# Performance work log

Measured on AMD Instinct MI355X. Metric: run time of the kernel, lower is better.

## Reference

```python
import jax, jax.numpy as jnp
import numpy as np

B, S, E = 4, 2048, 1024

def setup_inputs() -> dict:
    key = jax.random.key(0)
    ks = jax.random.split(key, 7)
    sc = 1.0 / np.sqrt(E)
    return {
        "x": jax.random.normal(ks[0], (B, S, E), dtype=jnp.float32),
        "wq_w": jax.random.normal(ks[1], (E, E), dtype=jnp.float32) * sc,
        "wq_b": jax.random.normal(ks[2], (E,), dtype=jnp.float32) * 0.01,
        "wk_w": jax.random.normal(ks[3], (E, E), dtype=jnp.float32) * sc,
        "wk_b": jax.random.normal(ks[4], (E,), dtype=jnp.float32) * 0.01,
        "wv_w": jax.random.normal(ks[5], (E, E), dtype=jnp.float32) * sc,
        "wv_b": jax.random.normal(ks[6], (E,), dtype=jnp.float32) * 0.01,
    }

def reference(x, wq_w, wq_b, wk_w, wk_b, wv_w, wv_b):
    # Linear projections (torch nn.Linear: y = x @ W^T + b)
    Q = jnp.einsum('bse,fe->bsf', x, wq_w) + wq_b
    K = jnp.einsum('bse,fe->bsf', x, wk_w) + wk_b
    V = jnp.einsum('bse,fe->bsf', x, wv_w) + wv_b
    # scaled dot-product attention, full [B, S, S] scores (single head)
    scores = jnp.einsum('bqe,bke->bqk', Q, K) / jnp.sqrt(jnp.asarray(Q.shape[-1], Q.dtype))
    attn = jax.nn.softmax(scores, axis=-1)
    return jnp.einsum('bqk,bke->bqe', attn, V)
```

## Files before the change

### kernel.cpp

```cpp
#include <hip/hip_runtime.h>
#include <hip/hip_bf16.h>
#include <stdint.h>

#define B_ 4
#define S_ 2048
#define E_ 1024

typedef __bf16 bf16;
typedef __attribute__((ext_vector_type(8))) __bf16 bf16x8;
typedef __attribute__((ext_vector_type(4))) float f32x4;
typedef __attribute__((ext_vector_type(4))) float float4v;
typedef __attribute__((ext_vector_type(4))) unsigned int uint4v;
typedef __attribute__((ext_vector_type(4))) unsigned short ushort4v;

__device__ inline unsigned short f2bf(float f) {
  union { float f; unsigned int u; } c; c.f = f;
  unsigned int u = c.u;
  unsigned int r = (u + 0x7FFFu + ((u >> 16) & 1u)) >> 16;
  return (unsigned short)r;
}

__device__ inline void load16_to_lds(const void* g, void* l) {
  __builtin_amdgcn_global_load_lds(
      (const __attribute__((address_space(1))) void*)g,
      (__attribute__((address_space(3))) void*)l,
      16, 0, 0);
}

__global__ __launch_bounds__(256) void cvt_all(
    const float* __restrict__ x, const float* __restrict__ w0,
    const float* __restrict__ w1, const float* __restrict__ w2,
    unsigned short* __restrict__ out) {
  const long off = (long)blockIdx.x * 256 + threadIdx.x;
  const float* in;
  long ibase;
  if (blockIdx.x < 8192)       { in = x;  ibase = 0; }
  else if (blockIdx.x < 9216)  { in = w0; ibase = 8192L * 256; }
  else if (blockIdx.x < 10240) { in = w1; ibase = 9216L * 256; }
  else                         { in = w2; ibase = 10240L * 256; }
  float4v f = ((const float4v*)in)[off - ibase];
  ushort4v o;
  o.x = f2bf(f.x); o.y = f2bf(f.y); o.z = f2bf(f.z); o.w = f2bf(f.w);
  ((ushort4v*)out)[off] = o;
}

template <int MODE, int SWZ, int NXT>
__global__ __launch_bounds__(256, 4) void gemm_bt(
    const bf16* __restrict__ A, const bf16* __restrict__ B, void* __restrict__ Cv,
    const float* __restrict__ bias, const float* __restrict__ bias_b,
    const float* __restrict__ bias_v, unsigned short* __restrict__ VtOut,
    float* __restrict__ rowsum,
    int M, int N, int K, int lda, int ldb, int ldc,
    long sA, long sB, long sC, float scale, int nyt) {
  __shared__ bf16 As[128 * 64];
  __shared__ bf16 Bs[128 * 64];

  int xt, yt, zb;
  if (SWZ == 0) {
    xt = blockIdx.x; yt = blockIdx.y; zb = blockIdx.z;
  } else {
    const int flat = blockIdx.x;
    const int xcd = flat & 7;
    const int local = flat >> 3;
    zb = xcd >> 1;
    const int w = (xcd & 1) * (NXT * nyt / 2) + local;
    xt = w % NXT; yt = w / NXT;
  }

  A += (long)zb * sA;
  B += (long)zb * sB;
  const int tid = threadIdx.x;
  const int wave = tid >> 6;
  const int lane = tid & 63;
  const int lrow = lane & 15;
  const int quad = lane >> 4;
  const int row0 = yt * 128;
  const int col0 = xt * 128;
  const int wm = (wave >> 1) * 64;
  const int wn = (wave & 1) * 64;

  f32x4 acc[4][4] = {};

  const int r0 = wave * 8 + (lane >> 3);
  const int c0 = (lane & 7) * 8;

  const bf16* pA0 = A + (long)(row0 + r0) * lda + c0;
  const bf16* pA1 = pA0 + 32L * lda;
  const bf16* pA2 = pA0 + 64L * lda;
  const bf16* pA3 = pA0 + 96L * lda;
  const bf16* pB0 = B + (long)(col0 + r0) * ldb + c0;
  const bf16* pB1 = pB0 + 32L * ldb;
  const bf16* pB2 = pB0 + 64L * ldb;
  const bf16* pB3 = pB0 + 96L * ldb;
  bf16* ldsA = As + wave * 512;
  bf16* ldsB = Bs + wave * 512;

  for (int ks = 0; ks < K; ks += 64) {
    load16_to_lds(pA0, ldsA);
    load16_to_lds(pA1, ldsA + 2048);
    load16_to_lds(pA2, ldsA + 4096);
    load16_to_lds(pA3, ldsA + 6144);
    load16_to_lds(pB0, ldsB);
    load16_to_lds(pB1, ldsB + 2048);
    load16_to_lds(pB2, ldsB + 4096);
    load16_to_lds(pB3, ldsB + 6144);
    __syncthreads();
#pragma unroll
    for (int kk = 0; kk < 64; kk += 32) {
      bf16x8 af[4], bfr[4];
#pragma unroll
      for (int i = 0; i < 4; ++i)
        af[i] = *(const bf16x8*)(As + (wm + i * 16 + lrow) * 64 + kk + quad * 8);
#pragma unroll
      for (int j = 0; j < 4; ++j)
        bfr[j] = *(const bf16x8*)(Bs + (wn + j * 16 + lrow) * 64 + kk + quad * 8);
#pragma unroll
      for (int i = 0; i < 4; ++i)
#pragma unroll
        for (int j = 0; j < 4; ++j)
          acc[i][j] = __builtin_amdgcn_mfma_f32_16x16x32_bf16(af[i], bfr[j], acc[i][j], 0, 0, 0);
    }
    __syncthreads();
    pA0 += 64; pA1 += 64; pA2 += 64; pA3 += 64;
    pB0 += 64; pB1 += 64; pB2 += 64; pB3 += 64;
  }

  if (MODE == 8) {
    float* C = (float*)Cv + (long)zb * sC;
    const float* rs = rowsum + (long)zb * S_;
#pragma unroll
    for (int i = 0; i < 4; ++i) {
#pragma unroll
      for (int r = 0; r < 4; ++r) {
        const int row = row0 + wm + i * 16 + quad * 4 + r;
        const float inv = 1.0f / rs[row];
#pragma unroll
        for (int j = 0; j < 4; ++j) {
          const int col = col0 + wn + j * 16 + lrow;
          C[(long)row * ldc + col] = acc[i][j][r] * inv;
        }
      }
    }
  } else if (MODE == 7) {
    unsigned short* C = (unsigned short*)Cv + (long)zb * sC;
    float* rs = rowsum + (long)zb * S_;
    float rsump[4][4];
#pragma unroll
    for (int i = 0; i < 4; ++i)
#pragma unroll
      for (int r = 0; r < 4; ++r) rsump[i][r] = 0.f;
#pragma unroll
    for (int j = 0; j < 4; ++j) {
      const int col = col0 + wn + j * 16 + lrow;
#pragma unroll
      for (int i = 0; i < 4; ++i) {
#pragma unroll
        for (int r = 0; r < 4; ++r) {
          const int row = row0 + wm + i * 16 + quad * 4 + r;
          const float e = __expf(acc[i][j][r] * scale);
          rsump[i][r] += e;
          C[(long)row * ldc + col] = f2bf(e);
        }
      }
    }
#pragma unroll
    for (int i = 0; i < 4; ++i) {
#pragma unroll
      for (int r = 0; r < 4; ++r) {
        float v = rsump[i][r];
        v += __shfl_xor(v, 1);
        v += __shfl_xor(v, 2);
        v += __shfl_xor(v, 4);
        v += __shfl_xor(v, 8);
        if (lrow == 0)
          atomicAdd(&rs[row0 + wm + i * 16 + quad * 4 + r], v);
      }
    }
  } else {
    if (col0 < 2048) {
      unsigned short* C = (unsigned short*)Cv;
#pragma unroll
      for (int j = 0; j < 4; ++j) {
        const int col = col0 + wn + j * 16 + lrow;
        const float bcol = (col < E_) ? bias[col] : bias_b[col - E_];
#pragma unroll
        for (int i = 0; i < 4; ++i) {
#pragma unroll
          for (int r = 0; r < 4; ++r) {
            const int row = row0 + wm + i * 16 + quad * 4 + r;
            C[(long)row * ldc + col] = f2bf(acc[i][j][r] + bcol);
          }
        }
      }
    } else {
#pragma unroll
      for (int j = 0; j < 4; ++j) {
        const int e = col0 + wn + j * 16 + lrow - 2048;
        const float bv_ = bias_v[e];
#pragma unroll
        for (int i = 0; i < 4; ++i) {
          const int row = row0 + wm + i * 16 + quad * 4;
          ushort4v o;
          o.x = f2bf(acc[i][j][0] + bv_);
          o.y = f2bf(acc[i][j][1] + bv_);
          o.z = f2bf(acc[i][j][2] + bv_);
          o.w = f2bf(acc[i][j][3] + bv_);
          *(ushort4v*)(VtOut + (long)e * (B_ * S_) + row) = o;
        }
      }
    }
  }
}

extern "C" void kernel_launch(void* const* d_in, const int* in_sizes, int n_in,
                              void* d_out, int out_size, void* d_ws, size_t ws_size,
                              hipStream_t stream) {
  const float* x    = (const float*)d_in[0];
  const float* wq_w = (const float*)d_in[1];
  const float* wq_b = (const float*)d_in[2];
  const float* wk_w = (const float*)d_in[3];
  const float* wk_b = (const float*)d_in[4];
  const float* wv_w = (const float*)d_in[5];
  const float* wv_b = (const float*)d_in[6];
  float* out = (float*)d_out;

  const long NX = (long)B_ * S_ * E_;
  const long NW = (long)E_ * E_;
  char* ws = (char*)d_ws;
  bf16* xb  = (bf16*)ws; ws += NX * 2;
  bf16* wqb = (bf16*)ws; ws += NW * 2;
  bf16* wkb = (bf16*)ws; ws += NW * 2;
  bf16* wvb = (bf16*)ws; ws += NW * 2;
  bf16* QK  = (bf16*)ws; ws += 2 * NX * 2;
  bf16* Vt  = (bf16*)ws; ws += NX * 2;
  bf16* Sc  = (bf16*)ws; ws += (long)B_ * S_ * S_ * 2;
  float* rowsum = (float*)ws; ws += (long)B_ * S_ * 4;

  cvt_all<<<dim3(11264), 256, 0, stream>>>(
      x, wq_w, wk_w, wv_w, (unsigned short*)xb);
  hipMemsetAsync(rowsum, 0, (size_t)B_ * S_ * 4, stream);

  dim3 blk(256);
  gemm_bt<6, 0, 24><<<dim3((3 * E_) / 128, (B_ * S_) / 128, 1), blk, 0, stream>>>(
      xb, wqb, QK, wq_b, wk_b, wv_b, (unsigned short*)Vt, nullptr,
      B_ * S_, 3 * E_, E_, E_, E_, 2 * E_, 0, 0, 0, 1.f, 64);
  gemm_bt<7, 1, 16><<<dim3(1024, 1, 1), blk, 0, stream>>>(
      QK, QK + E_, Sc, nullptr, nullptr, nullptr, nullptr, rowsum,
      S_, S_, E_, 2 * E_, 2 * E_, S_,
      (long)S_ * 2 * E_, (long)S_ * 2 * E_, (long)S_ * S_, 0.03125f, 16);
  gemm_bt<8, 1, 8><<<dim3(512, 1, 1), blk, 0, stream>>>(
      Sc, Vt, out, nullptr, nullptr, nullptr, nullptr, rowsum,
      S_, E_, S_, S_, B_ * S_, E_,
      (long)S_ * S_, (long)S_, (long)S_ * E_, 1.f, 16);
}
```

Baseline: 256.6 us.

## Add 256x256 double-buffered swizzled-LDS GEMM kernel for projection and score stages

Introduces a new 512-thread GEMM kernel with 256x256 output tiles, a 128KB double-buffered LDS with XOR swizzle, and a four-phase pipelined k-loop. Each phase issues the next global-to-LDS loads while running MFMAs, using explicit vmcnt waits, barriers and setprio. The QKV projection and QK^T score GEMMs now use it, while the PV GEMM stays on the old kernel. Larger tiles cut global traffic and the pipelining hides load latency, but the grids shrink to 384 and 256 blocks, which risks leaving CUs idle and lowers occupancy.

```diff
diff --git a/kernel.cpp b/kernel.cpp
--- a/kernel.cpp
+++ b/kernel.cpp
@@ -44,6 +44,237 @@
   ((ushort4v*)out)[off] = o;
 }
 
+
+#define MFMA_(a, b, c) __builtin_amdgcn_mfma_f32_16x16x32_bf16(a, b, c, 0, 0, 0)
+
+#define STAGE_A8(kh, buf, kofs)                                         \
+  { char* d_ = smem + (buf) * 65536 + (kh) * 16384 + wj;                \
+    load16_to_lds(pA0 + (kofs) + (kh) * 32, d_);                        \
+    load16_to_lds(pA1 + (kofs) + (kh) * 32, d_ + 1024); }
+
+#define STAGE_B8(kh, buf, kofs)                                         \
+  { char* d_ = smem + (buf) * 65536 + 32768 + (kh) * 16384 + wj;        \
+    load16_to_lds(pB0 + (kofs) + (kh) * 32, d_);                        \
+    load16_to_lds(pB1 + (kofs) + (kh) * 32, d_ + 1024); }
+
+#define PH_READS(mh, kh)                                                \
+    const char* rb_ = smem + cur * 65536 + (kh) * 16384;                \
+    bf16x8 a0_ = *(const bf16x8*)(rb_ + offA[(mh) * 4 + 0]);            \
+    bf16x8 a1_ = *(const bf16x8*)(rb_ + offA[(mh) * 4 + 1]);            \
+    bf16x8 a2_ = *(const bf16x8*)(rb_ + offA[(mh) * 4 + 2]);            \
+    bf16x8 a3_ = *(const bf16x8*)(rb_ + offA[(mh) * 4 + 3]);            \
+    bf16x8 b0_ = *(const bf16x8*)(rb_ + offB[0]);                       \
+    bf16x8 b1_ = *(const bf16x8*)(rb_ + offB[1]);                       \
+    bf16x8 b2_ = *(const bf16x8*)(rb_ + offB[2]);                       \
+    bf16x8 b3_ = *(const bf16x8*)(rb_ + offB[3])
+
+#define PH_TAIL(mh)                                                     \
+    __builtin_amdgcn_s_barrier();                                       \
+    asm volatile("s_waitcnt lgkmcnt(0)" ::: "memory");                  \
+    __builtin_amdgcn_s_setprio(1);                                      \
+    acc[(mh)*4+0][0] = MFMA_(a0_, b0_, acc[(mh)*4+0][0]);               \
+    acc[(mh)*4+0][1] = MFMA_(a0_, b1_, acc[(mh)*4+0][1]);               \
+    acc[(mh)*4+0][2] = MFMA_(a0_, b2_, acc[(mh)*4+0][2]);               \
+    acc[(mh)*4+0][3] = MFMA_(a0_, b3_, acc[(mh)*4+0][3]);               \
+    acc[(mh)*4+1][0] = MFMA_(a1_, b0_, acc[(mh)*4+1][0]);               \
+    acc[(mh)*4+1][1] = MFMA_(a1_, b1_, acc[(mh)*4+1][1]);               \
+    acc[(mh)*4+1][2] = MFMA_(a1_, b2_, acc[(mh)*4+1][2]);               \
+    acc[(mh)*4+1][3] = MFMA_(a1_, b3_, acc[(mh)*4+1][3]);               \
+    acc[(mh)*4+2][0] = MFMA_(a2_, b0_, acc[(mh)*4+2][0]);               \
+    acc[(mh)*4+2][1] = MFMA_(a2_, b1_, acc[(mh)*4+2][1]);               \
+    acc[(mh)*4+2][2] = MFMA_(a2_, b2_, acc[(mh)*4+2][2]);               \
+    acc[(mh)*4+2][3] = MFMA_(a2_, b3_, acc[(mh)*4+2][3]);               \
+    acc[(mh)*4+3][0] = MFMA_(a3_, b0_, acc[(mh)*4+3][0]);               \
+    acc[(mh)*4+3][1] = MFMA_(a3_, b1_, acc[(mh)*4+3][1]);               \
+    acc[(mh)*4+3][2] = MFMA_(a3_, b2_, acc[(mh)*4+3][2]);               \
+    acc[(mh)*4+3][3] = MFMA_(a3_, b3_, acc[(mh)*4+3][3]);               \
+    __builtin_amdgcn_s_setprio(0);                                      \
+    __builtin_amdgcn_s_barrier();
+
+template <int MODE>
+__global__ __launch_bounds__(512, 2) void gemm8(
+    const bf16* __restrict__ A, const bf16* __restrict__ B, void* __restrict__ Cv,
+    const float* __restrict__ bias, const float* __restrict__ bias_b,
+    const float* __restrict__ bias_v, unsigned short* __restrict__ VtOut,
+    float* __restrict__ rowsum,
+    int M, int N, int K, int lda, int ldb, int ldc,
+    long sA, long sB, long sC, float scale) {
+  (void)M; (void)N;
+  __shared__ __align__(128) char smem[131072];
+  const int tid = threadIdx.x;
+  const int wave = tid >> 6;
+  const int lane = tid & 63;
+  const int lrow = lane & 15;
+  const int quad = lane >> 4;
+  const int xt = blockIdx.x, yt = blockIdx.y, zb = blockIdx.z;
+  A += (long)zb * sA;
+  B += (long)zb * sB;
+  const int row0 = yt * 256;
+  const int col0 = xt * 256;
+  const int wm = (wave >> 2) * 128;
+  const int wn = (wave & 3) * 64;
+  const int wj = wave * 2048;
+
+  const bf16* pA0; const bf16* pA1; const bf16* pB0; const bf16* pB1;
+  {
+    int r0 = wave * 2048 + lane * 16;
+    int l0 = r0 ^ (((r0 >> 7) & 7) << 4);
+    int x0 = l0 >> 6;
+    int g0 = (l0 >> 4) & 3;
+    int r1 = r0 + 1024;
+    int l1 = r1 ^ (((r1 >> 7) & 7) << 4);
+    int x1 = l1 >> 6;
+    int g1 = (l1 >> 4) & 3;
+    pA0 = A + (long)(row0 + x0) * lda + g0 * 8;
+    pA1 = A + (long)(row0 + x1) * lda + g1 * 8;
+    pB0 = B + (long)(col0 + x0) * ldb + g0 * 8;
+    pB1 = B + (long)(col0 + x1) * ldb + g1 * 8;
+  }
+
+  int offA[8], offB[4];
+#pragma unroll
+  for (int mh = 0; mh < 2; ++mh)
+#pragma unroll
+    for (int f = 0; f < 4; ++f) {
+      int x = wm + mh * 64 + f * 16 + lrow;
+      int rb = ((x >> 1) << 7) + ((x & 1) << 6) + (quad << 4);
+      offA[mh * 4 + f] = rb ^ (((x >> 1) & 7) << 4);
+    }
+#pragma unroll
+  for (int n = 0; n < 4; ++n) {
+    int y = wn + n * 16 + lrow;
+    int rb = ((y >> 1) << 7) + ((y & 1) << 6) + (quad << 4);
+    offB[n] = (rb ^ (((y >> 1) & 7) << 4)) + 32768;
+  }
+
+  f32x4 acc[8][4] = {};
+  const int nt = K >> 6;
+
+  STAGE_A8(0, 0, 0); STAGE_B8(0, 0, 0);
+  STAGE_A8(1, 0, 0); STAGE_B8(1, 0, 0);
+  STAGE_A8(0, 1, 64); STAGE_B8(0, 1, 64);
+  asm volatile("s_waitcnt vmcnt(8)" ::: "memory");
+  __builtin_amdgcn_s_barrier();
+
+  for (int u = 0; u < nt; ++u) {
+    const int cur = u & 1;
+    const int nxt = cur ^ 1;
+    const int ks = u << 6;
+    const bool st1 = (u + 1 < nt);
+    const bool st2 = (u + 2 < nt);
+    {
+      PH_READS(0, 0);
+      if (st1) STAGE_A8(1, nxt, ks + 64);
+      PH_TAIL(0);
+    }
+    {
+      PH_READS(1, 0);
+      if (st1) STAGE_B8(1, nxt, ks + 64);
+      if (st1) { asm volatile("s_waitcnt vmcnt(8)" ::: "memory"); }
+      else     { asm volatile("s_waitcnt vmcnt(0)" ::: "memory"); }
+      PH_TAIL(1);
+    }
+    {
+      PH_READS(0, 1);
+      if (st2) STAGE_A8(0, cur, ks + 128);
+      PH_TAIL(0);
+    }
+    {
+      PH_READS(1, 1);
+      if (st2) STAGE_B8(0, cur, ks + 128);
+      if (st2)                 { asm volatile("s_waitcnt vmcnt(8)" ::: "memory"); }
+      else if (u == nt - 2)    { asm volatile("s_waitcnt vmcnt(4)" ::: "memory"); }
+      PH_TAIL(1);
+    }
+  }
+
+  if constexpr (MODE == 8) {
+    float* C = (float*)Cv + (long)zb * sC;
+    const float* rs = rowsum + (long)zb * S_;
+#pragma unroll
+    for (int m = 0; m < 8; ++m) {
+#pragma unroll
+      for (int r = 0; r < 4; ++r) {
+        const int row = row0 + wm + m * 16 + quad * 4 + r;
+        const float inv = 1.0f / rs[row];
+#pragma unroll
+        for (int n = 0; n < 4; ++n) {
+          const int col = col0 + wn + n * 16 + lrow;
+          C[(long)row * ldc + col] = acc[m][n][r] * inv;
+        }
+      }
+    }
+  } else if constexpr (MODE == 7) {
+    unsigned short* C = (unsigned short*)Cv + (long)zb * sC;
+    float* rs = rowsum + (long)zb * S_;
+    float rsump[8][4];
+#pragma unroll
+    for (int m = 0; m < 8; ++m)
+#pragma unroll
+      for (int r = 0; r < 4; ++r) rsump[m][r] = 0.f;
+#pragma unroll
+    for (int n = 0; n < 4; ++n) {
+      const int col = col0 + wn + n * 16 + lrow;
+#pragma unroll
+      for (int m = 0; m < 8; ++m) {
+#pragma unroll
+        for (int r = 0; r < 4; ++r) {
+          const int row = row0 + wm + m * 16 + quad * 4 + r;
+          const float e = __expf(acc[m][n][r] * scale);
+          rsump[m][r] += e;
+          C[(long)row * ldc + col] = f2bf(e);
+        }
+      }
+    }
+#pragma unroll
+    for (int m = 0; m < 8; ++m) {
+#pragma unroll
+      for (int r = 0; r < 4; ++r) {
+        float v = rsump[m][r];
+        v += __shfl_xor(v, 1);
+        v += __shfl_xor(v, 2);
+        v += __shfl_xor(v, 4);
+        v += __shfl_xor(v, 8);
+        if (lrow == 0)
+          atomicAdd(&rs[row0 + wm + m * 16 + quad * 4 + r], v);
+      }
+    }
+  } else {
+    if (col0 < 2048) {
+      unsigned short* C = (unsigned short*)Cv;
+#pragma unroll
+      for (int n = 0; n < 4; ++n) {
+        const int col = col0 + wn + n * 16 + lrow;
+        const float bcol = (col < E_) ? bias[col] : bias_b[col - E_];
+#pragma unroll
+        for (int m = 0; m < 8; ++m) {
+#pragma unroll
+          for (int r = 0; r < 4; ++r) {
+            const int row = row0 + wm + m * 16 + quad * 4 + r;
+            C[(long)row * ldc + col] = f2bf(acc[m][n][r] + bcol);
+          }
+        }
+      }
+    } else {
+#pragma unroll
+      for (int n = 0; n < 4; ++n) {
+        const int e = col0 + wn + n * 16 + lrow - 2048;
+        const float bv_ = bias_v[e];
+#pragma unroll
+        for (int m = 0; m < 8; ++m) {
+          const int row = row0 + wm + m * 16 + quad * 4;
+          ushort4v o;
+          o.x = f2bf(acc[m][n][0] + bv_);
+          o.y = f2bf(acc[m][n][1] + bv_);
+          o.z = f2bf(acc[m][n][2] + bv_);
+          o.w = f2bf(acc[m][n][3] + bv_);
+          *(ushort4v*)(VtOut + (long)e * (B_ * S_) + row) = o;
+        }
+      }
+    }
+  }
+}
+
 template <int MODE, int SWZ, int NXT>
 __global__ __launch_bounds__(256, 4) void gemm_bt(
     const bf16* __restrict__ A, const bf16* __restrict__ B, void* __restrict__ Cv,
@@ -240,14 +471,14 @@
       x, wq_w, wk_w, wv_w, (unsigned short*)xb);
   hipMemsetAsync(rowsum, 0, (size_t)B_ * S_ * 4, stream);
 
-  dim3 blk(256);
-  gemm_bt<6, 0, 24><<<dim3((3 * E_) / 128, (B_ * S_) / 128, 1), blk, 0, stream>>>(
+  gemm8<6><<<dim3(12, 32, 1), dim3(512), 0, stream>>>(
       xb, wqb, QK, wq_b, wk_b, wv_b, (unsigned short*)Vt, nullptr,
-      B_ * S_, 3 * E_, E_, E_, E_, 2 * E_, 0, 0, 0, 1.f, 64);
-  gemm_bt<7, 1, 16><<<dim3(1024, 1, 1), blk, 0, stream>>>(
+      B_ * S_, 3 * E_, E_, E_, E_, 2 * E_, 0, 0, 0, 1.f);
+  gemm8<7><<<dim3(8, 8, 4), dim3(512), 0, stream>>>(
       QK, QK + E_, Sc, nullptr, nullptr, nullptr, nullptr, rowsum,
       S_, S_, E_, 2 * E_, 2 * E_, S_,
-      (long)S_ * 2 * E_, (long)S_ * 2 * E_, (long)S_ * S_, 0.03125f, 16);
+      (long)S_ * 2 * E_, (long)S_ * 2 * E_, (long)S_ * S_, 0.03125f);
+  dim3 blk(256);
   gemm_bt<8, 1, 8><<<dim3(512, 1, 1), blk, 0, stream>>>(
       Sc, Vt, out, nullptr, nullptr, nullptr, nullptr, rowsum,
       S_, E_, S_, S_, B_ * S_, E_,
```

Measured after the change: 274.9 us. +7.1%, slower.
